# Kernel optimization log

Measured on AMD Instinct MI355X. Metric: run time of the kernel, lower is better.

Reference implementation:

```python
import jax, jax.numpy as jnp
import numpy as np

B, S, H, NH = 2, 2048, 2048, 16
DH = H // NH


def setup_inputs() -> dict:
    key = jax.random.key(0)
    ks = jax.random.split(key, 9)
    scale = 1.0 / np.sqrt(H)
    inp = {
        "hidden_state": jax.random.normal(ks[0], (B, S, H), dtype=jnp.float32),
        "Wq": jax.random.normal(ks[1], (H, H), dtype=jnp.float32) * scale,
        "bq": jnp.zeros((H,), dtype=jnp.float32),
        "Wk": jax.random.normal(ks[2], (H, H), dtype=jnp.float32) * scale,
        "bk": jnp.zeros((H,), dtype=jnp.float32),
        "Wv": jax.random.normal(ks[3], (H, H), dtype=jnp.float32) * scale,
        "bv": jnp.zeros((H,), dtype=jnp.float32),
        "Wo": jax.random.normal(ks[4], (H, H), dtype=jnp.float32) * scale,
        "bo": jnp.zeros((H,), dtype=jnp.float32),
    }
    # additive causal mask: 0 on/below diagonal, large negative above
    neg = jnp.float32(-1e9)
    tri = jnp.tril(jnp.ones((S, S), dtype=bool))
    inp["causal_mask"] = jnp.where(tri, 0.0, neg)[None, None, :, :]
    return inp


def reference(hidden_state, Wq, bq, Wk, bk, Wv, bv, Wo, bo, causal_mask):
    def split_heads(x):  # [B,S,H] -> [B,NH,S,DH]
        return x.reshape(B, S, NH, DH).transpose(0, 2, 1, 3)

    q = split_heads(hidden_state @ Wq + bq)
    k = split_heads(hidden_state @ Wk + bk)
    v = split_heads(hidden_state @ Wv + bv)

    scores = jnp.einsum("bhqd,bhkd->bhqk", q, k) / jnp.sqrt(jnp.float32(DH))
    scores = scores + causal_mask
    probs = jax.nn.softmax(scores, axis=-1)
    out = jnp.einsum("bhqk,bhkd->bhqd", probs, v)  # [B,NH,S,DH]
    out = out.transpose(0, 2, 1, 3).reshape(B, S, H)
    return out @ Wo + bo
```

## Files before the change

kernel.cpp:

```cpp
#include <hip/hip_runtime.h>
#include <cstdint>

typedef __attribute__((ext_vector_type(4))) float f32x4;
typedef __attribute__((ext_vector_type(8))) __bf16 bf16x8;
typedef __attribute__((ext_vector_type(4))) unsigned short u16x4;
typedef __attribute__((ext_vector_type(4))) float fvec4;

#define DEV __device__ __forceinline__
#define MFMA16(a, b, c) __builtin_amdgcn_mfma_f32_16x16x32_bf16((a), (b), (c), 0, 0, 0)

DEV unsigned short f2bf(float f) {
  union { float f; uint32_t u; } c; c.f = f;
  uint32_t u = c.u;
  return (unsigned short)((u + 0x7FFFu + ((u >> 16) & 1u)) >> 16);
}

DEV void gll16(const void* g, void* l) {
  __builtin_amdgcn_global_load_lds(
      (const __attribute__((address_space(1))) void*)(uintptr_t)g,
      (__attribute__((address_space(3))) void*)(uint32_t)(uintptr_t)l,
      16, 0, 0);
}

__global__ void cvt_bf16(const float* __restrict__ src, unsigned short* __restrict__ dst) {
  int i = (blockIdx.x * 256 + threadIdx.x) * 4;
  fvec4 v = *(const fvec4*)(src + i);
  u16x4 o;
  o[0] = f2bf(v[0]); o[1] = f2bf(v[1]); o[2] = f2bf(v[2]); o[3] = f2bf(v[3]);
  *(u16x4*)(dst + i) = o;
}

__global__ void transpose_cvt(const float* __restrict__ W, unsigned short* __restrict__ WT) {
  __shared__ float t[32][33];
  int n0 = blockIdx.x * 32, k0 = blockIdx.y * 32;
  int x = threadIdx.x, y = threadIdx.y;
  #pragma unroll
  for (int i = 0; i < 32; i += 8)
    t[y + i][x] = W[(size_t)(k0 + y + i) * 2048 + n0 + x];
  __syncthreads();
  #pragma unroll
  for (int i = 0; i < 32; i += 8)
    WT[(size_t)(n0 + y + i) * 2048 + k0 + x] = f2bf(t[x][y + i]);
}

template <int MODE>
__global__ __launch_bounds__(256, 2) void gemm128(
    const unsigned short* __restrict__ A,
    const unsigned short* __restrict__ Bt,
    const float* __restrict__ b0, const float* __restrict__ b1,
    const float* __restrict__ b2,
    void* __restrict__ o0, void* __restrict__ o1, void* __restrict__ o2) {
  __shared__ unsigned short As[128 * 64];
  __shared__ unsigned short Bs[128 * 64];
  const int n0 = blockIdx.x * 128, m0 = blockIdx.y * 128;
  const int tid = threadIdx.x;
  const int wave = tid >> 6, lid = tid & 63;
  const int l16 = lid & 15, lq = lid >> 4;
  const int wm = (wave >> 1) * 64, wn = (wave & 1) * 64;

  const int srow = lid >> 3;
  const int sgrp = (lid & 7) ^ srow;

  f32x4 acc[4][4] = {};

  for (int k0 = 0; k0 < 2048; k0 += 64) {
    #pragma unroll
    for (int i = 0; i < 4; ++i) {
      const int t = wave * 4 + i;
      const int r = t * 8 + srow;
      gll16(A + (size_t)(m0 + r) * 2048 + k0 + sgrp * 8, (char*)As + t * 1024 + lid * 16);
      gll16(Bt + (size_t)(n0 + r) * 2048 + k0 + sgrp * 8, (char*)Bs + t * 1024 + lid * 16);
    }
    __syncthreads();
    #pragma unroll
    for (int kk = 0; kk < 2; ++kk) {
      const int G = kk * 4 + lq;
      bf16x8 af[4], bfr[4];
      #pragma unroll
      for (int i = 0; i < 4; ++i)
        af[i] = *(const bf16x8*)(As + (wm + i * 16 + l16) * 64 + ((G ^ (l16 & 7)) << 3));
      #pragma unroll
      for (int j = 0; j < 4; ++j)
        bfr[j] = *(const bf16x8*)(Bs + (wn + j * 16 + l16) * 64 + ((G ^ (l16 & 7)) << 3));
      #pragma unroll
      for (int i = 0; i < 4; ++i)
        #pragma unroll
        for (int j = 0; j < 4; ++j)
          acc[i][j] = MFMA16(af[i], bfr[j], acc[i][j]);
    }
    __syncthreads();
  }

  #pragma unroll
  for (int j = 0; j < 4; ++j) {
    const int c = n0 + wn + j * 16 + l16;
    if (MODE == 1) {
      const int which = c >> 11;
      const int hd = c & 2047;
      const int h = hd >> 7, d = hd & 127;
      const float* bp = which == 0 ? b0 : which == 1 ? b1 : b2;
      const float bv = bp[hd];
      #pragma unroll
      for (int i = 0; i < 4; ++i) {
        #pragma unroll
        for (int r = 0; r < 4; ++r) {
          const int row = m0 + wm + i * 16 + lq * 4 + r;
          const int bb = row >> 11, s = row & 2047;
          const unsigned short us = f2bf(acc[i][j][r] + bv);
          const int bh = bb * 16 + h;
          if (which == 0)
            ((unsigned short*)o0)[(size_t)(bh * 2048 + s) * 128 + d] = us;
          else if (which == 1)
            ((unsigned short*)o1)[(size_t)(bh * 2048 + s) * 128 + d] = us;
          else
            ((unsigned short*)o2)[((size_t)(bh * 128 + d)) * 2048 + s] = us;
        }
      }
    } else {
      const float bv = b0[c];
      #pragma unroll
      for (int i = 0; i < 4; ++i)
        #pragma unroll
        for (int r = 0; r < 4; ++r) {
          const int row = m0 + wm + i * 16 + lq * 4 + r;
          ((float*)o0)[(size_t)row * 2048 + c] = acc[i][j][r] + bv;
        }
    }
  }
}

constexpr float SC = 0.08838834764831845f * 1.4426950408889634f;

__global__ __launch_bounds__(256, 2) void attn(
    const unsigned short* __restrict__ Q,
    const unsigned short* __restrict__ K,
    const unsigned short* __restrict__ Vt,
    unsigned short* __restrict__ ctx) {
  __shared__ unsigned short Ks[64 * 128];
  __shared__ unsigned short Vts[128 * 64];
  __shared__ unsigned short Ps[64 * 64];

  const int bh = blockIdx.y;
  const int b = bh >> 4, h = bh & 15;
  const unsigned short* Qh = Q + (size_t)bh * 2048 * 128;
  const unsigned short* Kh = K + (size_t)bh * 2048 * 128;
  const unsigned short* Vth = Vt + (size_t)bh * 128 * 2048;

  const int tid = threadIdx.x;
  const int wave = tid >> 6, lid = tid & 63;
  const int l16 = lid & 15, lq = lid >> 4;
  const int wq = wave * 16;

  for (int phase = 0; phase < 2; ++phase) {
    const int jq = phase == 0 ? (int)blockIdx.x : 31 - (int)blockIdx.x;
    const int q0 = jq * 64;

    bf16x8 qf[4];
    #pragma unroll
    for (int kc = 0; kc < 4; ++kc)
      qf[kc] = *(const bf16x8*)(Qh + (size_t)(q0 + wq + l16) * 128 + kc * 32 + lq * 8);

    float mrow[4], lrow[4];
    f32x4 acc_o[8];
    #pragma unroll
    for (int r = 0; r < 4; ++r) { mrow[r] = -1e30f; lrow[r] = 0.f; }
    #pragma unroll
    for (int dj = 0; dj < 8; ++dj) acc_o[dj] = (f32x4){0.f, 0.f, 0.f, 0.f};

    const int ntiles = jq + 1;
    for (int jt = 0; jt < ntiles; ++jt) {
      const int k0 = jt * 64;
      #pragma unroll
      for (int ii = 0; ii < 4; ++ii) {
        const int t = wave * 4 + ii;
        const int r = t * 4 + lq;
        const int g = l16 ^ (r & 15);
        gll16(Kh + (size_t)(k0 + r) * 128 + g * 8, (char*)Ks + t * 1024 + lid * 16);
      }
      #pragma unroll
      for (int ii = 0; ii < 4; ++ii) {
        const int t = wave * 4 + ii;
        const int d = t * 8 + (lid >> 3);
        const int g = (lid & 7) ^ (d & 7);
        gll16(Vth + (size_t)d * 2048 + k0 + g * 8, (char*)Vts + t * 1024 + lid * 16);
      }
      __syncthreads();

      f32x4 sacc[4] = {};
      #pragma unroll
      for (int kc = 0; kc < 4; ++kc) {
        #pragma unroll
        for (int jn = 0; jn < 4; ++jn) {
          bf16x8 kf = *(const bf16x8*)(Ks + (jn * 16 + l16) * 128 + (((kc * 4 + lq) ^ l16) << 3));
          sacc[jn] = MFMA16(qf[kc], kf, sacc[jn]);
        }
      }

      const bool diag = (jt == ntiles - 1);
      #pragma unroll
      for (int r = 0; r < 4; ++r) {
        const int ql = wq + lq * 4 + r;
        const int qrow = q0 + ql;
        float sv[4];
        float tmax = -1e30f;
        #pragma unroll
        for (int jn = 0; jn < 4; ++jn) {
          float s = sacc[jn][r] * SC;
          if (diag && (k0 + jn * 16 + l16 > qrow)) s = -1e30f;
          sv[jn] = s;
          tmax = fmaxf(tmax, s);
        }
        tmax = fmaxf(tmax, __shfl_xor(tmax, 1));
        tmax = fmaxf(tmax, __shfl_xor(tmax, 2));
        tmax = fmaxf(tmax, __shfl_xor(tmax, 4));
        tmax = fmaxf(tmax, __shfl_xor(tmax, 8));
        const float mnew = fmaxf(mrow[r], tmax);
        const float alpha = exp2f(mrow[r] - mnew);
        mrow[r] = mnew;
        float psum = 0.f;
        #pragma unroll
        for (int jn = 0; jn < 4; ++jn) {
          const float p = exp2f(sv[jn] - mnew);
          psum += p;
          const int sg = (jn * 2 + (l16 >> 3)) ^ (ql & 7);
          Ps[ql * 64 + (sg << 3) + (l16 & 7)] = f2bf(p);
        }
        psum += __shfl_xor(psum, 1);
        psum += __shfl_xor(psum, 2);
        psum += __shfl_xor(psum, 4);
        psum += __shfl_xor(psum, 8);
        lrow[r] = lrow[r] * alpha + psum;
        #pragma unroll
        for (int dj = 0; dj < 8; ++dj) acc_o[dj][r] *= alpha;
      }
      __syncthreads();

      #pragma unroll
      for (int kc = 0; kc < 2; ++kc) {
        const int G = kc * 4 + lq;
        bf16x8 pf = *(const bf16x8*)(Ps + (wq + l16) * 64 + ((G ^ (l16 & 7)) << 3));
        #pragma unroll
        for (int dj = 0; dj < 8; ++dj) {
          bf16x8 vf = *(const bf16x8*)(Vts + (dj * 16 + l16) * 64 + ((G ^ (l16 & 7)) << 3));
          acc_o[dj] = MFMA16(pf, vf, acc_o[dj]);
        }
      }
      __syncthreads();
    }

    #pragma unroll
    for (int r = 0; r < 4; ++r) {
      const int s = q0 + wq + lq * 4 + r;
      const float inv = 1.f / lrow[r];
      const size_t base = ((size_t)(b * 2048 + s)) * 2048 + h * 128;
      #pragma unroll
      for (int dj = 0; dj < 8; ++dj)
        ctx[base + dj * 16 + l16] = f2bf(acc_o[dj][r] * inv);
    }
  }
}

extern "C" void kernel_launch(void* const* d_in, const int* in_sizes, int n_in,
                              void* d_out, int out_size, void* d_ws, size_t ws_size,
                              hipStream_t stream) {
  const float* hs = (const float*)d_in[0];
  const float* Wq = (const float*)d_in[1];
  const float* bq = (const float*)d_in[2];
  const float* Wk = (const float*)d_in[3];
  const float* bk = (const float*)d_in[4];
  const float* Wv = (const float*)d_in[5];
  const float* bv = (const float*)d_in[6];
  const float* Wo = (const float*)d_in[7];
  const float* bo = (const float*)d_in[8];
  float* out = (float*)d_out;

  char* ws = (char*)d_ws;
  unsigned short* hsb   = (unsigned short*)(ws);
  unsigned short* wqkvt = (unsigned short*)(ws + (16 << 20));
  unsigned short* wot   = (unsigned short*)(ws + (40 << 20));
  unsigned short* Qb    = (unsigned short*)(ws + (48 << 20));
  unsigned short* Kb    = (unsigned short*)(ws + (64 << 20));
  unsigned short* Vtb   = (unsigned short*)(ws + (80 << 20));
  unsigned short* ctx   = (unsigned short*)(ws + (96 << 20));

  cvt_bf16<<<dim3(8192), dim3(256), 0, stream>>>(hs, hsb);
  dim3 tb(32, 8);
  transpose_cvt<<<dim3(64, 64), tb, 0, stream>>>(Wq, wqkvt);
  transpose_cvt<<<dim3(64, 64), tb, 0, stream>>>(Wk, wqkvt + 2048 * 2048);
  transpose_cvt<<<dim3(64, 64), tb, 0, stream>>>(Wv, wqkvt + 2 * 2048 * 2048);
  transpose_cvt<<<dim3(64, 64), tb, 0, stream>>>(Wo, wot);

  gemm128<1><<<dim3(48, 32), 256, 0, stream>>>(hsb, wqkvt, bq, bk, bv,
                                               (void*)Qb, (void*)Kb, (void*)Vtb);
  attn<<<dim3(16, 32), 256, 0, stream>>>(Qb, Kb, Vtb, ctx);
  gemm128<0><<<dim3(16, 32), 256, 0, stream>>>(ctx, wot, bo, nullptr, nullptr,
                                               (void*)out, nullptr, nullptr);
}
```

Measured before the change: 455.8 us.

## Restructure attention to transposed S^T MFMA layout, one q-tile per block

The attention kernel now computes S^T = K·Q^T, so each lane owns one query row. Row max and sum reductions need only two cross-lane shuffles, and P is written to LDS as packed vectors. The softmax scale is folded into Q inside the QKV GEMM epilogue. Each block now handles one query tile with a 32-wide grid and launch_bounds raised to 4, replacing the paired-tile balancing scheme. V^T stores become vectorised, and the four weight transposes merge into one launch. The risks are load imbalance from dropping the paired causal tiles, and register pressure at the higher occupancy target.

```diff
diff --git a/kernel.cpp b/kernel.cpp
--- a/kernel.cpp
+++ b/kernel.cpp
@@ -30,8 +30,12 @@
   *(u16x4*)(dst + i) = o;
 }
 
-__global__ void transpose_cvt(const float* __restrict__ W, unsigned short* __restrict__ WT) {
+__global__ void transpose_cvt4(const float* __restrict__ W0, const float* __restrict__ W1,
+                               const float* __restrict__ W2, const float* __restrict__ W3,
+                               unsigned short* __restrict__ Dqkv, unsigned short* __restrict__ Do) {
   __shared__ float t[32][33];
+  const float* W = blockIdx.z == 0 ? W0 : blockIdx.z == 1 ? W1 : blockIdx.z == 2 ? W2 : W3;
+  unsigned short* WT = blockIdx.z < 3 ? Dqkv + (size_t)blockIdx.z * 2048 * 2048 : Do;
   int n0 = blockIdx.x * 32, k0 = blockIdx.y * 32;
   int x = threadIdx.x, y = threadIdx.y;
   #pragma unroll
@@ -42,6 +46,8 @@
   for (int i = 0; i < 32; i += 8)
     WT[(size_t)(n0 + y + i) * 2048 + k0 + x] = f2bf(t[x][y + i]);
 }
+
+constexpr float QSC = 0.08838834764831845f * 1.4426950408889634f;
 
 template <int MODE>
 __global__ __launch_bounds__(256, 2) void gemm128(
@@ -100,20 +106,27 @@
       const int h = hd >> 7, d = hd & 127;
       const float* bp = which == 0 ? b0 : which == 1 ? b1 : b2;
       const float bv = bp[hd];
-      #pragma unroll
-      for (int i = 0; i < 4; ++i) {
-        #pragma unroll
-        for (int r = 0; r < 4; ++r) {
-          const int row = m0 + wm + i * 16 + lq * 4 + r;
-          const int bb = row >> 11, s = row & 2047;
-          const unsigned short us = f2bf(acc[i][j][r] + bv);
-          const int bh = bb * 16 + h;
-          if (which == 0)
-            ((unsigned short*)o0)[(size_t)(bh * 2048 + s) * 128 + d] = us;
-          else if (which == 1)
-            ((unsigned short*)o1)[(size_t)(bh * 2048 + s) * 128 + d] = us;
-          else
-            ((unsigned short*)o2)[((size_t)(bh * 128 + d)) * 2048 + s] = us;
+      if (which == 2) {
+        #pragma unroll
+        for (int i = 0; i < 4; ++i) {
+          const int row0 = m0 + wm + i * 16 + lq * 4;
+          const int bb = row0 >> 11, s0 = row0 & 2047;
+          u16x4 pv;
+          #pragma unroll
+          for (int r = 0; r < 4; ++r) pv[r] = f2bf(acc[i][j][r] + bv);
+          *(u16x4*)((unsigned short*)o2 + ((size_t)((bb * 16 + h) * 128 + d)) * 2048 + s0) = pv;
+        }
+      } else {
+        const float sc = which == 0 ? QSC : 1.0f;
+        unsigned short* op = which == 0 ? (unsigned short*)o0 : (unsigned short*)o1;
+        #pragma unroll
+        for (int i = 0; i < 4; ++i) {
+          #pragma unroll
+          for (int r = 0; r < 4; ++r) {
+            const int row = m0 + wm + i * 16 + lq * 4 + r;
+            const int bb = row >> 11, s = row & 2047;
+            op[(size_t)((bb * 16 + h) * 2048 + s) * 128 + d] = f2bf((acc[i][j][r] + bv) * sc);
+          }
         }
       }
     } else {
@@ -129,9 +142,7 @@
   }
 }
 
-constexpr float SC = 0.08838834764831845f * 1.4426950408889634f;
-
-__global__ __launch_bounds__(256, 2) void attn(
+__global__ __launch_bounds__(256, 4) void attn(
     const unsigned short* __restrict__ Q,
     const unsigned short* __restrict__ K,
     const unsigned short* __restrict__ Vt,
@@ -140,6 +151,8 @@
   __shared__ unsigned short Vts[128 * 64];
   __shared__ unsigned short Ps[64 * 64];
 
+  const int jq = 31 - (int)blockIdx.x;
+  const int q0 = jq * 64;
   const int bh = blockIdx.y;
   const int b = bh >> 4, h = bh & 15;
   const unsigned short* Qh = Q + (size_t)bh * 2048 * 128;
@@ -150,113 +163,109 @@
   const int wave = tid >> 6, lid = tid & 63;
   const int l16 = lid & 15, lq = lid >> 4;
   const int wq = wave * 16;
-
-  for (int phase = 0; phase < 2; ++phase) {
-    const int jq = phase == 0 ? (int)blockIdx.x : 31 - (int)blockIdx.x;
-    const int q0 = jq * 64;
-
-    bf16x8 qf[4];
-    #pragma unroll
-    for (int kc = 0; kc < 4; ++kc)
-      qf[kc] = *(const bf16x8*)(Qh + (size_t)(q0 + wq + l16) * 128 + kc * 32 + lq * 8);
-
-    float mrow[4], lrow[4];
-    f32x4 acc_o[8];
-    #pragma unroll
-    for (int r = 0; r < 4; ++r) { mrow[r] = -1e30f; lrow[r] = 0.f; }
-    #pragma unroll
-    for (int dj = 0; dj < 8; ++dj) acc_o[dj] = (f32x4){0.f, 0.f, 0.f, 0.f};
-
-    const int ntiles = jq + 1;
-    for (int jt = 0; jt < ntiles; ++jt) {
-      const int k0 = jt * 64;
-      #pragma unroll
-      for (int ii = 0; ii < 4; ++ii) {
-        const int t = wave * 4 + ii;
-        const int r = t * 4 + lq;
-        const int g = l16 ^ (r & 15);
-        gll16(Kh + (size_t)(k0 + r) * 128 + g * 8, (char*)Ks + t * 1024 + lid * 16);
+  const int ql = wq + l16;
+  const int qrow = q0 + ql;
+  const int sw = 2 * (l16 & 7);
+
+  bf16x8 qf[4];
+  #pragma unroll
+  for (int kc = 0; kc < 4; ++kc)
+    qf[kc] = *(const bf16x8*)(Qh + (size_t)qrow * 128 + kc * 32 + lq * 8);
+
+  float m_i = -1e30f, l_i = 0.f;
+  f32x4 acc[8] = {};
+
+  for (int jt = 0; jt <= jq; ++jt) {
+    const int k0 = jt * 64;
+    #pragma unroll
+    for (int ii = 0; ii < 4; ++ii) {
+      const int t = wave * 4 + ii;
+      const int r = t * 4 + lq;
+      const int g = l16 ^ (r & 15);
+      gll16(Kh + (size_t)(k0 + r) * 128 + g * 8, (char*)Ks + t * 1024 + lid * 16);
+    }
+    #pragma unroll
+    for (int ii = 0; ii < 4; ++ii) {
+      const int t = wave * 4 + ii;
+      const int d = t * 8 + (lid >> 3);
+      const int g = (lid & 7) ^ (d & 7);
+      gll16(Vth + (size_t)d * 2048 + k0 + g * 8, (char*)Vts + t * 1024 + lid * 16);
+    }
+    __syncthreads();
+
+    f32x4 sacc[4] = {};
+    #pragma unroll
+    for (int kc = 0; kc < 4; ++kc) {
+      #pragma unroll
+      for (int km = 0; km < 4; ++km) {
+        bf16x8 af = *(const bf16x8*)(Ks + (km * 16 + l16) * 128 + (((kc * 4 + lq) ^ l16) << 3));
+        sacc[km] = MFMA16(af, qf[kc], sacc[km]);
       }
-      #pragma unroll
-      for (int ii = 0; ii < 4; ++ii) {
-        const int t = wave * 4 + ii;
-        const int d = t * 8 + (lid >> 3);
-        const int g = (lid & 7) ^ (d & 7);
-        gll16(Vth + (size_t)d * 2048 + k0 + g * 8, (char*)Vts + t * 1024 + lid * 16);
+    }
+
+    if (jt == jq) {
+      #pragma unroll
+      for (int km = 0; km < 4; ++km)
+        #pragma unroll
+        for (int r = 0; r < 4; ++r)
+          if (k0 + km * 16 + lq * 4 + r > qrow) sacc[km][r] = -1e30f;
+    }
+
+    float tmax = -1e30f;
+    #pragma unroll
+    for (int km = 0; km < 4; ++km)
+      #pragma unroll
+      for (int r = 0; r < 4; ++r) tmax = fmaxf(tmax, sacc[km][r]);
+    tmax = fmaxf(tmax, __shfl_xor(tmax, 16));
+    tmax = fmaxf(tmax, __shfl_xor(tmax, 32));
+
+    const float mnew = fmaxf(m_i, tmax);
+    const float alpha = exp2f(m_i - mnew);
+    m_i = mnew;
+
+    float ps = 0.f;
+    u16x4 pk[4];
+    #pragma unroll
+    for (int km = 0; km < 4; ++km) {
+      #pragma unroll
+      for (int r = 0; r < 4; ++r) {
+        const float p = exp2f(sacc[km][r] - mnew);
+        ps += p;
+        pk[km][r] = f2bf(p);
       }
-      __syncthreads();
-
-      f32x4 sacc[4] = {};
-      #pragma unroll
-      for (int kc = 0; kc < 4; ++kc) {
-        #pragma unroll
-        for (int jn = 0; jn < 4; ++jn) {
-          bf16x8 kf = *(const bf16x8*)(Ks + (jn * 16 + l16) * 128 + (((kc * 4 + lq) ^ l16) << 3));
-          sacc[jn] = MFMA16(qf[kc], kf, sacc[jn]);
-        }
+    }
+    ps += __shfl_xor(ps, 16);
+    ps += __shfl_xor(ps, 32);
+    l_i = l_i * alpha + ps;
+    #pragma unroll
+    for (int dm = 0; dm < 8; ++dm) acc[dm] *= alpha;
+
+    #pragma unroll
+    for (int km = 0; km < 4; ++km)
+      *(u16x4*)(Ps + ql * 64 + ((((km * 4) + lq) ^ sw) << 2)) = pk[km];
+
+    #pragma unroll
+    for (int kc = 0; kc < 2; ++kc) {
+      const int G = kc * 4 + lq;
+      const int pg = (kc * 8 + 2 * lq) ^ sw;
+      bf16x8 pf = *(const bf16x8*)(Ps + ql * 64 + (pg << 2));
+      #pragma unroll
+      for (int dm = 0; dm < 8; ++dm) {
+        bf16x8 vf = *(const bf16x8*)(Vts + (dm * 16 + l16) * 64 + ((G ^ (l16 & 7)) << 3));
+        acc[dm] = MFMA16(vf, pf, acc[dm]);
       }
-
-      const bool diag = (jt == ntiles - 1);
-      #pragma unroll
-      for (int r = 0; r < 4; ++r) {
-        const int ql = wq + lq * 4 + r;
-        const int qrow = q0 + ql;
-        float sv[4];
-        float tmax = -1e30f;
-        #pragma unroll
-        for (int jn = 0; jn < 4; ++jn) {
-          float s = sacc[jn][r] * SC;
-          if (diag && (k0 + jn * 16 + l16 > qrow)) s = -1e30f;
-          sv[jn] = s;
-          tmax = fmaxf(tmax, s);
-        }
-        tmax = fmaxf(tmax, __shfl_xor(tmax, 1));
-        tmax = fmaxf(tmax, __shfl_xor(tmax, 2));
-        tmax = fmaxf(tmax, __shfl_xor(tmax, 4));
-        tmax = fmaxf(tmax, __shfl_xor(tmax, 8));
-        const float mnew = fmaxf(mrow[r], tmax);
-        const float alpha = exp2f(mrow[r] - mnew);
-        mrow[r] = mnew;
-        float psum = 0.f;
-        #pragma unroll
-        for (int jn = 0; jn < 4; ++jn) {
-          const float p = exp2f(sv[jn] - mnew);
-          psum += p;
-          const int sg = (jn * 2 + (l16 >> 3)) ^ (ql & 7);
-          Ps[ql * 64 + (sg << 3) + (l16 & 7)] = f2bf(p);
-        }
-        psum += __shfl_xor(psum, 1);
-        psum += __shfl_xor(psum, 2);
-        psum += __shfl_xor(psum, 4);
-        psum += __shfl_xor(psum, 8);
-        lrow[r] = lrow[r] * alpha + psum;
-        #pragma unroll
-        for (int dj = 0; dj < 8; ++dj) acc_o[dj][r] *= alpha;
-      }
-      __syncthreads();
-
-      #pragma unroll
-      for (int kc = 0; kc < 2; ++kc) {
-        const int G = kc * 4 + lq;
-        bf16x8 pf = *(const bf16x8*)(Ps + (wq + l16) * 64 + ((G ^ (l16 & 7)) << 3));
-        #pragma unroll
-        for (int dj = 0; dj < 8; ++dj) {
-          bf16x8 vf = *(const bf16x8*)(Vts + (dj * 16 + l16) * 64 + ((G ^ (l16 & 7)) << 3));
-          acc_o[dj] = MFMA16(pf, vf, acc_o[dj]);
-        }
-      }
-      __syncthreads();
-    }
-
-    #pragma unroll
-    for (int r = 0; r < 4; ++r) {
-      const int s = q0 + wq + lq * 4 + r;
-      const float inv = 1.f / lrow[r];
-      const size_t base = ((size_t)(b * 2048 + s)) * 2048 + h * 128;
-      #pragma unroll
-      for (int dj = 0; dj < 8; ++dj)
-        ctx[base + dj * 16 + l16] = f2bf(acc_o[dj][r] * inv);
-    }
+    }
+    __syncthreads();
+  }
+
+  const float inv = 1.f / l_i;
+  const size_t base = ((size_t)(b * 2048 + qrow)) * 2048 + h * 128;
+  #pragma unroll
+  for (int dm = 0; dm < 8; ++dm) {
+    u16x4 o;
+    #pragma unroll
+    for (int r = 0; r < 4; ++r) o[r] = f2bf(acc[dm][r] * inv);
+    *(u16x4*)(ctx + base + dm * 16 + lq * 4) = o;
   }
 }
 
@@ -284,15 +293,11 @@
   unsigned short* ctx   = (unsigned short*)(ws + (96 << 20));
 
   cvt_bf16<<<dim3(8192), dim3(256), 0, stream>>>(hs, hsb);
-  dim3 tb(32, 8);
-  transpose_cvt<<<dim3(64, 64), tb, 0, stream>>>(Wq, wqkvt);
-  transpose_cvt<<<dim3(64, 64), tb, 0, stream>>>(Wk, wqkvt + 2048 * 2048);
-  transpose_cvt<<<dim3(64, 64), tb, 0, stream>>>(Wv, wqkvt + 2 * 2048 * 2048);
-  transpose_cvt<<<dim3(64, 64), tb, 0, stream>>>(Wo, wot);
+  transpose_cvt4<<<dim3(64, 64, 4), dim3(32, 8), 0, stream>>>(Wq, Wk, Wv, Wo, wqkvt, wot);
 
   gemm128<1><<<dim3(48, 32), 256, 0, stream>>>(hsb, wqkvt, bq, bk, bv,
                                                (void*)Qb, (void*)Kb, (void*)Vtb);
-  attn<<<dim3(16, 32), 256, 0, stream>>>(Qb, Kb, Vtb, ctx);
+  attn<<<dim3(32, 32), 256, 0, stream>>>(Qb, Kb, Vtb, ctx);
   gemm128<0><<<dim3(16, 32), 256, 0, stream>>>(ctx, wot, bo, nullptr, nullptr,
                                                (void*)out, nullptr, nullptr);
 }
```

New measurement: 410.5 us. -9.9%, faster.
